# Performance work log

Measured on AMD Instinct MI355X. Metric: run time of the kernel, lower is better.

Reference implementation:

```python
import jax, jax.numpy as jnp
import numpy as np

KS = 7  # transform conv kernel size


def setup_inputs() -> dict:
    key = jax.random.key(0)
    kx, kq, kk, kv, kt = jax.random.split(key, 5)
    b, c, h, w = 4, 64, 64, 64
    x = jax.random.normal(kx, (b, c, h, w), dtype=jnp.float32)
    # 1x1 convs (out_channel=1, bias=False) -> weight vectors over channels
    q_w = jax.random.normal(kq, (c,), dtype=jnp.float32) * 0.05
    k_w = jax.random.normal(kk, (c,), dtype=jnp.float32) * 0.05
    v_w = jax.random.normal(kv, (c,), dtype=jnp.float32) * 0.05
    # transform conv: 1 -> 1 channel, 7x7, reflect pad, no bias
    t_w = jax.random.normal(kt, (1, 1, KS, KS), dtype=jnp.float32) * 0.05
    return {"x": x, "q_w": q_w, "k_w": k_w, "v_w": v_w, "t_w": t_w}


def reference(x, q_w, k_w, v_w, t_w):
    b, c, h, w = x.shape
    hw = h * w
    # 1x1 convs to single channel, flattened over spatial dims -> [b, HW]
    q = jnp.einsum('bchw,c->bhw', x, q_w).reshape(b, hw)
    k = jnp.einsum('bchw,c->bhw', x, k_w).reshape(b, hw)
    v = jnp.einsum('bchw,c->bhw', x, v_w).reshape(b, hw)
    # degenerate head_dim=1 attention: scores are an outer product [b, HW, HW]
    scores = q[:, :, None] * k[:, None, :]
    attn_w = jax.nn.softmax(scores, axis=-1)
    attn = jnp.einsum('bij,bj->bi', attn_w, v).reshape(b, 1, h, w)
    # transform: reflect-pad then 7x7 valid conv
    pad = KS // 2
    attn_p = jnp.pad(attn, ((0, 0), (0, 0), (pad, pad), (pad, pad)), mode='reflect')
    out = jax.lax.conv_general_dilated(
        attn_p, t_w, window_strides=(1, 1), padding='VALID',
        dimension_numbers=('NCHW', 'OIHW', 'NCHW'))
    return out
```

## Files before the change

kernel.cpp:

```cpp
#include <hip/hip_runtime.h>

#define C 64
#define HW 4096
#define NM 20
#define SIGQ 0x7E3A91D4u
#define SIGM 0x5C1B72E8u
#define PSTRIDE 112
#define PBASE 4096

__device__ __constant__ float INVF[NM] = {
    1.0000000000e+00f, 1.0000000000e+00f, 5.0000000000e-01f, 1.6666666667e-01f,
    4.1666666667e-02f, 8.3333333333e-03f, 1.3888888889e-03f, 1.9841269841e-04f,
    2.4801587302e-05f, 2.7557319224e-06f, 2.7557319224e-07f, 2.5052108385e-08f,
    2.0876756988e-09f, 1.6059043837e-10f, 1.1470745598e-11f, 7.6471637318e-13f,
    4.7794773324e-14f, 2.8114572543e-15f, 1.5619206968e-16f, 8.2206352466e-18f
};

__device__ __forceinline__ void st_rlx(uint32_t* p, uint32_t v) {
    __hip_atomic_store(p, v, __ATOMIC_RELAXED, __HIP_MEMORY_SCOPE_AGENT);
}
__device__ __forceinline__ uint32_t ld_rlx(const uint32_t* p) {
    return __hip_atomic_load(p, __ATOMIC_RELAXED, __HIP_MEMORY_SCOPE_AGENT);
}

__global__ __launch_bounds__(64) void fused_kernel(
    const float* __restrict__ x,
    const float* __restrict__ qw,
    const float* __restrict__ kw,
    const float* __restrict__ vw,
    const float* __restrict__ tw,
    float* __restrict__ out,
    uint32_t* __restrict__ W) {
    __shared__ float red[64 * 41];
    __shared__ float cf[2 * NM];
    __shared__ float attn_s[7 * 64];
    __shared__ float wgt[49];

    const int lane = threadIdx.x;
    const int bl = blockIdx.x;
    const int b = bl >> 6, y = bl & 63;

    uint32_t* qflags = W;
    uint32_t* mflags = W + 256;
    uint32_t* part = W + PBASE + bl * PSTRIDE;

    const float* xb = x + ((size_t)b * C) * HW + y * 64 + lane;
    float qa = 0.f, ka = 0.f, va = 0.f;
#pragma unroll
    for (int c = 0; c < C; ++c) {
        float xv = xb[(size_t)c * HW];
        qa = fmaf(xv, qw[c], qa);
        ka = fmaf(xv, kw[c], ka);
        va = fmaf(xv, vw[c], va);
    }
    st_rlx(part + 40 + lane, __float_as_uint(qa));
    asm volatile("s_waitcnt vmcnt(0)" ::: "memory");
    if (lane == 0) st_rlx(qflags + bl, SIGQ);

    {
        float t = 1.f;
#pragma unroll
        for (int m = 0; m < NM; ++m) {
            red[lane * 41 + m] = t;
            red[lane * 41 + NM + m] = t * va;
            t *= ka;
        }
    }
    if (lane < 49) wgt[lane] = tw[lane];
    __syncthreads();
    if (lane < 2 * NM) {
        float s = 0.f;
#pragma unroll
        for (int i = 0; i < 64; ++i) s += red[i * 41 + lane];
        s *= INVF[lane < NM ? lane : lane - NM];
        st_rlx(part + lane, __float_as_uint(s));
    }
    asm volatile("s_waitcnt vmcnt(0)" ::: "memory");
    if (lane == 0) st_rlx(mflags + bl, SIGM);

    {
        const uint32_t* f = qflags + b * 64 + lane;
        bool done = false;
        int guard = 0;
        while (true) {
            if (!done) done = (ld_rlx(f) == SIGQ);
            if (__all(done)) break;
            if (++guard > (1 << 16)) break;
            __builtin_amdgcn_s_sleep(1);
        }
        asm volatile("" ::: "memory");
    }
    uint32_t qt[7];
#pragma unroll
    for (int o = 0; o < 7; ++o) {
        if (o == 3) continue;
        int r = y + o - 3;
        r = r < 0 ? -r : (r > 63 ? 126 - r : r);
        qt[o] = ld_rlx(W + PBASE + (b * 64 + r) * PSTRIDE + 40 + lane);
    }

    {
        const uint32_t* f = mflags + b * 64 + lane;
        bool done = false;
        int guard = 0;
        while (true) {
            if (!done) done = (ld_rlx(f) == SIGM);
            if (__all(done)) break;
            if (++guard > (1 << 16)) break;
            __builtin_amdgcn_s_sleep(1);
        }
        asm volatile("" ::: "memory");
    }

    uint32_t t[64];
    const uint32_t* pb = W + PBASE + (b * 64) * PSTRIDE + lane;
#pragma unroll
    for (int p = 0; p < 64; ++p) t[p] = ld_rlx(pb + p * PSTRIDE);
    {
        float f[64];
#pragma unroll
        for (int p = 0; p < 64; ++p) f[p] = __uint_as_float(t[p]);
#pragma unroll
        for (int st = 1; st < 64; st <<= 1)
#pragma unroll
            for (int i = 0; i < 64; i += 2 * st) f[i] += f[i + st];
        if (lane < 2 * NM) cf[lane] = f[0];
    }
    __syncthreads();

#pragma unroll
    for (int o = 0; o < 7; ++o) {
        float qv = (o == 3) ? qa : __uint_as_float(qt[o]);
        float ng = cf[NM - 1], nf = cf[2 * NM - 1];
#pragma unroll
        for (int mm = NM - 2; mm >= 0; --mm) {
            ng = fmaf(ng, qv, cf[mm]);
            nf = fmaf(nf, qv, cf[NM + mm]);
        }
        attn_s[o * 64 + lane] = nf / ng;
    }
    __syncthreads();

    float acc = 0.f;
#pragma unroll
    for (int dy = 0; dy < 7; ++dy) {
#pragma unroll
        for (int dx = 0; dx < 7; ++dx) {
            int xx = lane + dx - 3;
            xx = xx < 0 ? -xx : (xx > 63 ? 126 - xx : xx);
            acc = fmaf(attn_s[dy * 64 + xx], wgt[dy * 7 + dx], acc);
        }
    }
    out[(size_t)b * HW + y * 64 + lane] = acc;
}

extern "C" void kernel_launch(void* const* d_in, const int* in_sizes, int n_in,
                              void* d_out, int out_size, void* d_ws, size_t ws_size,
                              hipStream_t stream) {
    const float* x  = (const float*)d_in[0];
    const float* qw = (const float*)d_in[1];
    const float* kw = (const float*)d_in[2];
    const float* vw = (const float*)d_in[3];
    const float* tw = (const float*)d_in[4];
    float* out = (float*)d_out;
    uint32_t* W = (uint32_t*)d_ws;

    fused_kernel<<<256, 64, 0, stream>>>(x, qw, kw, vw, tw, out, W);
}
```

Before: 13.73 us.

## Process four rows per block with 64 blocks of 256 threads

Regroups the work so each block handles four image rows with four waves, giving 64 blocks instead of 256. Each batch now has 16 producer blocks instead of 64, which cuts the number of flags to poll and the partial sums to reduce in the cross-block spin-wait. Halo q rows are staged in LDS so neighbouring rows computed inside the block are reused rather than reloaded. The trade-off is fewer blocks to spread across CUs plus extra intra-block syncs and an LDS reduction across waves.

```diff
diff --git a/kernel.cpp b/kernel.cpp
--- a/kernel.cpp
+++ b/kernel.cpp
@@ -5,7 +5,7 @@
 #define NM 20
 #define SIGQ 0x7E3A91D4u
 #define SIGM 0x5C1B72E8u
-#define PSTRIDE 112
+#define PSTRIDE 304
 #define PBASE 4096
 
 __device__ __constant__ float INVF[NM] = {
@@ -23,7 +23,11 @@
     return __hip_atomic_load(p, __ATOMIC_RELAXED, __HIP_MEMORY_SCOPE_AGENT);
 }
 
-__global__ __launch_bounds__(64) void fused_kernel(
+__device__ __forceinline__ int reflect64(int r) {
+    return r < 0 ? -r : (r > 63 ? 126 - r : r);
+}
+
+__global__ __launch_bounds__(256) void fused_kernel(
     const float* __restrict__ x,
     const float* __restrict__ qw,
     const float* __restrict__ kw,
@@ -31,20 +35,26 @@
     const float* __restrict__ tw,
     float* __restrict__ out,
     uint32_t* __restrict__ W) {
-    __shared__ float red[64 * 41];
+    __shared__ float red[256 * 41];
+    __shared__ float wred[4][41];
     __shared__ float cf[2 * NM];
-    __shared__ float attn_s[7 * 64];
+    __shared__ float q_lds[10][64];
+    __shared__ float attn_s[10][64];
     __shared__ float wgt[49];
 
-    const int lane = threadIdx.x;
+    const int tid = threadIdx.x;
+    const int lane = tid & 63;
+    const int wv = tid >> 6;
     const int bl = blockIdx.x;
-    const int b = bl >> 6, y = bl & 63;
+    const int b = bl >> 4;
+    const int g = bl & 15;
+    const int col = lane;
 
     uint32_t* qflags = W;
-    uint32_t* mflags = W + 256;
+    uint32_t* mflags = W + 64;
     uint32_t* part = W + PBASE + bl * PSTRIDE;
 
-    const float* xb = x + ((size_t)b * C) * HW + y * 64 + lane;
+    const float* xb = x + ((size_t)b * C) * HW + g * 256 + tid;
     float qa = 0.f, ka = 0.f, va = 0.f;
 #pragma unroll
     for (int c = 0; c < C; ++c) {
@@ -53,34 +63,41 @@
         ka = fmaf(xv, kw[c], ka);
         va = fmaf(xv, vw[c], va);
     }
-    st_rlx(part + 40 + lane, __float_as_uint(qa));
+    st_rlx(part + 40 + tid, __float_as_uint(qa));
     asm volatile("s_waitcnt vmcnt(0)" ::: "memory");
-    if (lane == 0) st_rlx(qflags + bl, SIGQ);
+    __syncthreads();
+    if (tid == 0) st_rlx(qflags + bl, SIGQ);
 
     {
         float t = 1.f;
 #pragma unroll
         for (int m = 0; m < NM; ++m) {
-            red[lane * 41 + m] = t;
-            red[lane * 41 + NM + m] = t * va;
+            red[tid * 41 + m] = t;
+            red[tid * 41 + NM + m] = t * va;
             t *= ka;
         }
     }
-    if (lane < 49) wgt[lane] = tw[lane];
+    if (tid < 49) wgt[tid] = tw[tid];
     __syncthreads();
     if (lane < 2 * NM) {
         float s = 0.f;
 #pragma unroll
-        for (int i = 0; i < 64; ++i) s += red[i * 41 + lane];
-        s *= INVF[lane < NM ? lane : lane - NM];
-        st_rlx(part + lane, __float_as_uint(s));
+        for (int i = 0; i < 64; ++i) s += red[(wv * 64 + i) * 41 + lane];
+        wred[wv][lane] = s;
+    }
+    __syncthreads();
+    if (tid < 2 * NM) {
+        float s = ((wred[0][tid] + wred[1][tid]) + (wred[2][tid] + wred[3][tid]));
+        s *= INVF[tid < NM ? tid : tid - NM];
+        st_rlx(part + tid, __float_as_uint(s));
     }
     asm volatile("s_waitcnt vmcnt(0)" ::: "memory");
-    if (lane == 0) st_rlx(mflags + bl, SIGM);
-
-    {
-        const uint32_t* f = qflags + b * 64 + lane;
-        bool done = false;
+    __syncthreads();
+    if (tid == 0) st_rlx(mflags + bl, SIGM);
+
+    if (wv == 0) {
+        const uint32_t* f = qflags + b * 16 + lane;
+        bool done = (lane >= 16);
         int guard = 0;
         while (true) {
             if (!done) done = (ld_rlx(f) == SIGQ);
@@ -90,18 +107,29 @@
         }
         asm volatile("" ::: "memory");
     }
-    uint32_t qt[7];
-#pragma unroll
-    for (int o = 0; o < 7; ++o) {
-        if (o == 3) continue;
-        int r = y + o - 3;
-        r = r < 0 ? -r : (r > 63 ? 126 - r : r);
-        qt[o] = ld_rlx(W + PBASE + (b * 64 + r) * PSTRIDE + 40 + lane);
-    }
+    __syncthreads();
+
+    q_lds[3 + wv][col] = qa;
 
     {
-        const uint32_t* f = mflags + b * 64 + lane;
-        bool done = false;
+        int pA = (wv < 3) ? wv : 7;
+        int rowA = reflect64(4 * g - 3 + pA);
+        uint32_t hA = ld_rlx(W + PBASE + (b * 16 + (rowA >> 2)) * PSTRIDE +
+                             40 + (rowA & 3) * 64 + col);
+        uint32_t hB = 0;
+        int pB = 8 + wv;
+        if (wv < 2) {
+            int rowB = reflect64(4 * g - 3 + pB);
+            hB = ld_rlx(W + PBASE + (b * 16 + (rowB >> 2)) * PSTRIDE +
+                        40 + (rowB & 3) * 64 + col);
+        }
+        q_lds[pA][col] = __uint_as_float(hA);
+        if (wv < 2) q_lds[pB][col] = __uint_as_float(hB);
+    }
+
+    if (wv == 0) {
+        const uint32_t* f = mflags + b * 16 + lane;
+        bool done = (lane >= 16);
         int guard = 0;
         while (true) {
             if (!done) done = (ld_rlx(f) == SIGM);
@@ -110,34 +138,37 @@
             __builtin_amdgcn_s_sleep(1);
         }
         asm volatile("" ::: "memory");
-    }
-
-    uint32_t t[64];
-    const uint32_t* pb = W + PBASE + (b * 64) * PSTRIDE + lane;
-#pragma unroll
-    for (int p = 0; p < 64; ++p) t[p] = ld_rlx(pb + p * PSTRIDE);
-    {
-        float f[64];
-#pragma unroll
-        for (int p = 0; p < 64; ++p) f[p] = __uint_as_float(t[p]);
-#pragma unroll
-        for (int st = 1; st < 64; st <<= 1)
-#pragma unroll
-            for (int i = 0; i < 64; i += 2 * st) f[i] += f[i + st];
-        if (lane < 2 * NM) cf[lane] = f[0];
-    }
-    __syncthreads();
-
-#pragma unroll
-    for (int o = 0; o < 7; ++o) {
-        float qv = (o == 3) ? qa : __uint_as_float(qt[o]);
-        float ng = cf[NM - 1], nf = cf[2 * NM - 1];
-#pragma unroll
-        for (int mm = NM - 2; mm >= 0; --mm) {
-            ng = fmaf(ng, qv, cf[mm]);
-            nf = fmaf(nf, qv, cf[NM + mm]);
-        }
-        attn_s[o * 64 + lane] = nf / ng;
+        if (lane < 2 * NM) {
+            uint32_t t[16];
+            const uint32_t* pb = W + PBASE + (b * 16) * PSTRIDE + lane;
+#pragma unroll
+            for (int p = 0; p < 16; ++p) t[p] = ld_rlx(pb + p * PSTRIDE);
+            float fs[16];
+#pragma unroll
+            for (int p = 0; p < 16; ++p) fs[p] = __uint_as_float(t[p]);
+#pragma unroll
+            for (int st = 1; st < 16; st <<= 1)
+#pragma unroll
+                for (int i = 0; i < 16; i += 2 * st) fs[i] += fs[i + st];
+            cf[lane] = fs[0];
+        }
+    }
+    __syncthreads();
+
+#pragma unroll
+    for (int pass = 0; pass < 3; ++pass) {
+        int s = pass * 256 + tid;
+        int o = s >> 6, cc = s & 63;
+        if (o < 10) {
+            float qv = q_lds[o][cc];
+            float ng = cf[NM - 1], nf = cf[2 * NM - 1];
+#pragma unroll
+            for (int mm = NM - 2; mm >= 0; --mm) {
+                ng = fmaf(ng, qv, cf[mm]);
+                nf = fmaf(nf, qv, cf[NM + mm]);
+            }
+            attn_s[o][cc] = nf / ng;
+        }
     }
     __syncthreads();
 
@@ -146,12 +177,12 @@
     for (int dy = 0; dy < 7; ++dy) {
 #pragma unroll
         for (int dx = 0; dx < 7; ++dx) {
-            int xx = lane + dx - 3;
+            int xx = col + dx - 3;
             xx = xx < 0 ? -xx : (xx > 63 ? 126 - xx : xx);
-            acc = fmaf(attn_s[dy * 64 + xx], wgt[dy * 7 + dx], acc);
-        }
-    }
-    out[(size_t)b * HW + y * 64 + lane] = acc;
+            acc = fmaf(attn_s[wv + dy][xx], wgt[dy * 7 + dx], acc);
+        }
+    }
+    out[(size_t)b * HW + (4 * g + wv) * 64 + col] = acc;
 }
 
 extern "C" void kernel_launch(void* const* d_in, const int* in_sizes, int n_in,
@@ -165,5 +196,5 @@
     float* out = (float*)d_out;
     uint32_t* W = (uint32_t*)d_ws;
 
-    fused_kernel<<<256, 64, 0, stream>>>(x, qw, kw, vw, tw, out, W);
-}
+    fused_kernel<<<64, 256, 0, stream>>>(x, qw, kw, vw, tw, out, W);
+}
```

Result: faster. 12.71 us (-7.5%).
